# Kernel tuning notes

Hardware: AMD Instinct MI355X
Metric: run time of the kernel (lower is better)

## Reference

```python
import jax, jax.numpy as jnp
import numpy as np

T = 4096          # total packed tokens
SEG = 512         # segment length (position_ids reset every SEG)
D = 768           # hidden_size
H = 12            # num_attention_heads
DH = D // H       # head_dim = 64
THETA = 160000.0  # global_rope_theta (layer_id=0 -> global attention)


def setup_inputs() -> dict:
    key = jax.random.key(0)
    k1, k2, k3 = jax.random.split(key, 3)
    hidden_states = jax.random.normal(k1, (T, D), dtype=jnp.float32)
    # torch Linear weights stored transposed: here [in, out] for x @ W
    Wqkv = jax.random.normal(k2, (D, 3 * D), dtype=jnp.float32) / np.sqrt(D).astype(np.float32)
    Wo = jax.random.normal(k3, (D, D), dtype=jnp.float32) / np.sqrt(D).astype(np.float32)
    # packed batch: 8 segments of length SEG, position ids restart at 0
    position_ids = (jnp.arange(T, dtype=jnp.int32) % SEG)
    return {"hidden_states": hidden_states, "Wqkv": Wqkv, "Wo": Wo,
            "position_ids": position_ids}


def _neox_rope(x, pos):
    # x: [T, H, DH]; neox-style rotary over full head_dim
    half = DH // 2
    inv_freq = 1.0 / (THETA ** (jnp.arange(half, dtype=jnp.float32) * 2.0 / DH))
    freqs = pos.astype(jnp.float32)[:, None] * inv_freq[None, :]   # [T, half]
    cos = jnp.cos(freqs)[:, None, :]                               # [T, 1, half]
    sin = jnp.sin(freqs)[:, None, :]
    x1, x2 = x[..., :half], x[..., half:]
    return jnp.concatenate([x1 * cos - x2 * sin, x2 * cos + x1 * sin], axis=-1)


def reference(hidden_states, Wqkv, Wo, position_ids):
    qkv = hidden_states @ Wqkv                         # [T, 3D]
    q, k, v = jnp.split(qkv, 3, axis=-1)
    q = q.reshape(T, H, DH)
    k = k.reshape(T, H, DH)
    v = v.reshape(T, H, DH)
    q = _neox_rope(q, position_ids)
    k = _neox_rope(k, position_ids)
    # segment id per token (position_ids==0 marks a new sequence)
    seg = jnp.cumsum((position_ids == 0).astype(jnp.int32)) - 1
    mask = seg[:, None] == seg[None, :]                # block-diagonal [T, T]
    scale = 1.0 / np.sqrt(DH).astype(np.float32)
    scores = jnp.einsum('thd,shd->hts', q, k) * scale  # [H, T, T]
    scores = jnp.where(mask[None, :, :], scores, jnp.float32(-1e30))
    attn = jax.nn.softmax(scores, axis=-1)
    out = jnp.einsum('hts,shd->thd', attn, v).reshape(T, D)
    return out @ Wo
```

## Files before the change

kernel.cpp:

```cpp
#include <hip/hip_runtime.h>
#include <hip/hip_bf16.h>
#include <math.h>

#define T_TOK 4096
#define D_MODEL 768
#define H_HEADS 12
#define DH 64
#define SEG 512
#define NSEG 8
#define QKV_LD 2304

typedef __bf16 bf16x8_t __attribute__((ext_vector_type(8)));
typedef float f32x4_t __attribute__((ext_vector_type(4)));
typedef float f32x16_t __attribute__((ext_vector_type(16)));

#define GBK 64
#define QSCALE 0.18033688011112042f

#define FENCED_BARRIER()                         \
    do {                                         \
        __builtin_amdgcn_sched_barrier(0);       \
        __builtin_amdgcn_s_barrier();            \
        __builtin_amdgcn_sched_barrier(0);       \
    } while (0)

__device__ __forceinline__ void tconv_body(const float* __restrict__ in,
                                           __hip_bfloat16* __restrict__ out,
                                           int N, int K, int bx, int by, int tid,
                                           float (*tile)[65]) {
    const int k0 = by * 64;
    const int n0 = bx * 64;
    const int rr = tid >> 4;
    const int cc = (tid & 15) * 4;
#pragma unroll
    for (int i = 0; i < 4; ++i) {
        int r = i * 16 + rr;
        float4 v = *(const float4*)(in + (size_t)(k0 + r) * N + n0 + cc);
        tile[r][cc] = v.x; tile[r][cc + 1] = v.y; tile[r][cc + 2] = v.z; tile[r][cc + 3] = v.w;
    }
    __syncthreads();
#pragma unroll
    for (int i = 0; i < 4; ++i) {
        int n = i * 16 + rr;
        union { __hip_bfloat16 h[4]; ushort4 u; } o;
        o.h[0] = __float2bfloat16(tile[cc + 0][n]);
        o.h[1] = __float2bfloat16(tile[cc + 1][n]);
        o.h[2] = __float2bfloat16(tile[cc + 2][n]);
        o.h[3] = __float2bfloat16(tile[cc + 3][n]);
        *(ushort4*)(out + (size_t)(n0 + n) * K + k0 + cc) = o.u;
    }
}

__global__ __launch_bounds__(256) void prep_inputs(const float* __restrict__ hidden,
                                                   const float* __restrict__ Wqkv,
                                                   const float* __restrict__ Wo,
                                                   const int* __restrict__ pos_ids,
                                                   __hip_bfloat16* __restrict__ Xb,
                                                   __hip_bfloat16* __restrict__ Wqkvt,
                                                   __hip_bfloat16* __restrict__ Wot,
                                                   float2* __restrict__ rtab) {
    __shared__ float tile[64][65];
    const int b = blockIdx.x;
    const int tid = threadIdx.x;
    if (b < 3072) {
        int i = b * 256 + tid;
        float4 v = ((const float4*)hidden)[i];
        union { __hip_bfloat16 h[4]; ushort4 u; } o;
        o.h[0] = __float2bfloat16(v.x); o.h[1] = __float2bfloat16(v.y);
        o.h[2] = __float2bfloat16(v.z); o.h[3] = __float2bfloat16(v.w);
        ((ushort4*)Xb)[i] = o.u;
    } else if (b < 3504) {
        int lb = b - 3072;
        tconv_body(Wqkv, Wqkvt, QKV_LD, D_MODEL, lb % 36, lb / 36, tid, tile);
    } else if (b < 3648) {
        int lb = b - 3504;
        tconv_body(Wo, Wot, D_MODEL, D_MODEL, lb % 12, lb / 12, tid, tile);
    } else {
        int idx = (b - 3648) * 256 + tid;
        int t = idx >> 5;
        int i = idx & 31;
        float pos = (float)pos_ids[t];
        float inv_freq = powf(160000.0f, -(float)i / 32.0f);
        float s, c;
        sincosf(pos * inv_freq, &s, &c);
        rtab[idx] = make_float2(c, s);
    }
}

__global__ __launch_bounds__(512) void gemm_qkv_fused(const __hip_bfloat16* __restrict__ A,
                                                      const __hip_bfloat16* __restrict__ Bt,
                                                      const float2* __restrict__ rtab,
                                                      __hip_bfloat16* __restrict__ Qb,
                                                      __hip_bfloat16* __restrict__ Kb,
                                                      __hip_bfloat16* __restrict__ Vtb) {
    __shared__ __hip_bfloat16 As[2][128 * GBK];
    __shared__ __hip_bfloat16 Bs[2][128 * GBK];
    const int tid = threadIdx.x;
    const int lane = tid & 63;
    const int wid = tid >> 6;
    const int wr = wid >> 1;
    const int wc = wid & 1;
    const int orig = blockIdx.y * 18 + blockIdx.x;
    const int wg = (orig & 7) * 72 + (orig >> 3);
    const int m0 = (wg / 18) * 128;
    const int n0 = (wg % 18) * 128;
    const int K = D_MODEL;

    f32x4_t acc[2][4];
#pragma unroll
    for (int i = 0; i < 2; ++i)
#pragma unroll
        for (int j = 0; j < 4; ++j) acc[i][j] = (f32x4_t){0.f, 0.f, 0.f, 0.f};

    const int lr = lane >> 3;
    const int gc = lane & 7;
    const int swzc = (gc ^ lr) << 3;
    const int fr = lane & 15;
    const int l4 = lane >> 4;
    const int fsw = fr & 7;

#define STAGE_Q(buf_, k0_)                                                            \
    do {                                                                              \
        _Pragma("unroll")                                                             \
        for (int i_ = 0; i_ < 2; ++i_) {                                              \
            const int row_ = i_ * 64 + wid * 8;                                       \
            const __hip_bfloat16* ga_ = A + (size_t)(m0 + row_ + lr) * K + (k0_) + swzc; \
            __builtin_amdgcn_global_load_lds(                                         \
                (const __attribute__((address_space(1))) void*)ga_,                   \
                (__attribute__((address_space(3))) void*)(As[buf_] + row_ * GBK), 16, 0, 0); \
            const __hip_bfloat16* gb_ = Bt + (size_t)(n0 + row_ + lr) * K + (k0_) + swzc; \
            __builtin_amdgcn_global_load_lds(                                         \
                (const __attribute__((address_space(1))) void*)gb_,                   \
                (__attribute__((address_space(3))) void*)(Bs[buf_] + row_ * GBK), 16, 0, 0); \
        }                                                                             \
    } while (0)

    const int NKT = K / GBK;
    STAGE_Q(0, 0);
    for (int kt = 0; kt < NKT; ++kt) {
        const int cur = kt & 1;
        if (kt < NKT - 1) {
            STAGE_Q(cur ^ 1, (kt + 1) * GBK);
            asm volatile("s_waitcnt vmcnt(4)" ::: "memory");
        } else {
            asm volatile("s_waitcnt vmcnt(0)" ::: "memory");
        }
        FENCED_BARRIER();
#pragma unroll
        for (int kk = 0; kk < 2; ++kk) {
            const int rg = ((kk * 4 + l4) ^ fsw) << 3;
            bf16x8_t af[2], bfr[4];
#pragma unroll
            for (int mi = 0; mi < 2; ++mi)
                af[mi] = *(const bf16x8_t*)(As[cur] + (wr * 32 + mi * 16 + fr) * GBK + rg);
#pragma unroll
            for (int ni = 0; ni < 4; ++ni)
                bfr[ni] = *(const bf16x8_t*)(Bs[cur] + (wc * 64 + ni * 16 + fr) * GBK + rg);
#pragma unroll
            for (int mi = 0; mi < 2; ++mi)
#pragma unroll
                for (int ni = 0; ni < 4; ++ni)
                    acc[mi][ni] = __builtin_amdgcn_mfma_f32_16x16x32_bf16(
                        af[mi], bfr[ni], acc[mi][ni], 0, 0, 0);
        }
        asm volatile("" ::: "memory");
        FENCED_BARRIER();
    }
#undef STAGE_Q

    const int colbase = n0 + wc * 64;
    const int chunk = colbase >> 6;
    const int part = chunk / H_HEADS;
    const int h = chunk % H_HEADS;
    const int trow0 = m0 + wr * 32;

    ushort* scr = ((wid < 4) ? (ushort*)As : (ushort*)Bs) + (wid & 3) * 2560;

    if (part == 2) {
        const int seg = trow0 >> 9;
        const int key0 = trow0 & 511;
#pragma unroll
        for (int mi = 0; mi < 2; ++mi)
#pragma unroll
            for (int ni = 0; ni < 4; ++ni) {
                int d = ni * 16 + fr;
#pragma unroll
                for (int j = 0; j < 4; ++j)
                    scr[d * 40 + mi * 16 + l4 * 4 + j] =
                        __bfloat16_as_ushort(__float2bfloat16(acc[mi][ni][j]));
            }
        __builtin_amdgcn_sched_barrier(0);
        const ushort* rp = scr + lane * 40;
        uint4 v0 = *(const uint4*)(rp);
        uint4 v1 = *(const uint4*)(rp + 8);
        uint4 v2 = *(const uint4*)(rp + 16);
        uint4 v3 = *(const uint4*)(rp + 24);
        __hip_bfloat16* vd = Vtb + ((size_t)(h * NSEG + seg) * DH + lane) * SEG + key0;
        ((uint4*)vd)[0] = v0; ((uint4*)vd)[1] = v1;
        ((uint4*)vd)[2] = v2; ((uint4*)vd)[3] = v3;
    } else {
        __hip_bfloat16* dst = (part == 0) ? Qb : Kb;
        const float scale = (part == 0) ? QSCALE : 1.0f;
#pragma unroll
        for (int mi = 0; mi < 2; ++mi)
#pragma unroll
            for (int j = 0; j < 4; ++j) {
                int rl = mi * 16 + l4 * 4 + j;
                int t = trow0 + rl;
                const float2* tb = rtab + (size_t)t * 32;
                float2 cs0 = tb[fr];
                float2 cs1 = tb[16 + fr];
                float x1, x2;
                x1 = acc[mi][0][j]; x2 = acc[mi][2][j];
                scr[rl * 72 + fr] =
                    __bfloat16_as_ushort(__float2bfloat16((x1 * cs0.x - x2 * cs0.y) * scale));
                scr[rl * 72 + 32 + fr] =
                    __bfloat16_as_ushort(__float2bfloat16((x2 * cs0.x + x1 * cs0.y) * scale));
                x1 = acc[mi][1][j]; x2 = acc[mi][3][j];
                scr[rl * 72 + 16 + fr] =
                    __bfloat16_as_ushort(__float2bfloat16((x1 * cs1.x - x2 * cs1.y) * scale));
                scr[rl * 72 + 48 + fr] =
                    __bfloat16_as_ushort(__float2bfloat16((x2 * cs1.x + x1 * cs1.y) * scale));
            }
        __builtin_amdgcn_sched_barrier(0);
        const int row = lane >> 1, half = lane & 1;
        const ushort* rp = scr + row * 72 + half * 32;
        uint4 a0 = *(const uint4*)(rp);
        uint4 a1 = *(const uint4*)(rp + 8);
        uint4 a2 = *(const uint4*)(rp + 16);
        uint4 a3 = *(const uint4*)(rp + 24);
        __hip_bfloat16* op = dst + ((size_t)h * T_TOK + trow0 + row) * DH + half * 32;
        ((uint4*)op)[0] = a0; ((uint4*)op)[1] = a1;
        ((uint4*)op)[2] = a2; ((uint4*)op)[3] = a3;
    }
}

__global__ __launch_bounds__(256) void gemm_wo64(const __hip_bfloat16* __restrict__ A,
                                                 const __hip_bfloat16* __restrict__ Bt,
                                                 float* __restrict__ C) {
    __shared__ __hip_bfloat16 As[2][64 * GBK];
    __shared__ __hip_bfloat16 Bs[2][64 * GBK];
    const int tid = threadIdx.x;
    const int lane = tid & 63;
    const int wid = tid >> 6;
    const int wr = wid >> 1, wc = wid & 1;
    const int orig = blockIdx.y * 12 + blockIdx.x;
    const int wg = (orig & 7) * 96 + (orig >> 3);
    const int m0 = (wg / 12) * 64;
    const int n0 = (wg % 12) * 64;
    const int K = D_MODEL;
    const int N = D_MODEL;

    f32x4_t acc[2][2];
#pragma unroll
    for (int i = 0; i < 2; ++i)
#pragma unroll
        for (int j = 0; j < 2; ++j) acc[i][j] = (f32x4_t){0.f, 0.f, 0.f, 0.f};

    const int lr = lane >> 3;
    const int gc = lane & 7;
    const int swzc = (gc ^ lr) << 3;
    const int fr = lane & 15;
    const int l4 = lane >> 4;
    const int fsw = fr & 7;

#define STAGE_W(buf_, k0_)                                                            \
    do {                                                                              \
        _Pragma("unroll")                                                             \
        for (int i_ = 0; i_ < 2; ++i_) {                                              \
            const int row_ = i_ * 32 + wid * 8;                                       \
            const __hip_bfloat16* ga_ = A + (size_t)(m0 + row_ + lr) * K + (k0_) + swzc; \
            __builtin_amdgcn_global_load_lds(                                         \
                (const __attribute__((address_space(1))) void*)ga_,                   \
                (__attribute__((address_space(3))) void*)(As[buf_] + row_ * GBK), 16, 0, 0); \
            const __hip_bfloat16* gb_ = Bt + (size_t)(n0 + row_ + lr) * K + (k0_) + swzc; \
            __builtin_amdgcn_global_load_lds(                                         \
                (const __attribute__((address_space(1))) void*)gb_,                   \
                (__attribute__((address_space(3))) void*)(Bs[buf_] + row_ * GBK), 16, 0, 0); \
        }                                                                             \
    } while (0)

    const int NKT = K / GBK;
    STAGE_W(0, 0);
    for (int kt = 0; kt < NKT; ++kt) {
        const int cur = kt & 1;
        if (kt < NKT - 1) {
            STAGE_W(cur ^ 1, (kt + 1) * GBK);
            asm volatile("s_waitcnt vmcnt(4)" ::: "memory");
        } else {
            asm volatile("s_waitcnt vmcnt(0)" ::: "memory");
        }
        FENCED_BARRIER();
#pragma unroll
        for (int kk = 0; kk < 2; ++kk) {
            const int rg = ((kk * 4 + l4) ^ fsw) << 3;
            bf16x8_t af[2], bfr[2];
#pragma unroll
            for (int mi = 0; mi < 2; ++mi)
                af[mi] = *(const bf16x8_t*)(As[cur] + (wr * 32 + mi * 16 + fr) * GBK + rg);
#pragma unroll
            for (int ni = 0; ni < 2; ++ni)
                bfr[ni] = *(const bf16x8_t*)(Bs[cur] + (wc * 32 + ni * 16 + fr) * GBK + rg);
#pragma unroll
            for (int mi = 0; mi < 2; ++mi)
#pragma unroll
                for (int ni = 0; ni < 2; ++ni)
                    acc[mi][ni] = __builtin_amdgcn_mfma_f32_16x16x32_bf16(
                        af[mi], bfr[ni], acc[mi][ni], 0, 0, 0);
        }
        asm volatile("" ::: "memory");
        FENCED_BARRIER();
    }
#undef STAGE_W

    float* Cb = C + (size_t)(m0 + wr * 32) * N + n0 + wc * 32;
#pragma unroll
    for (int mi = 0; mi < 2; ++mi)
#pragma unroll
        for (int ni = 0; ni < 2; ++ni)
#pragma unroll
            for (int j = 0; j < 4; ++j) {
                int r = mi * 16 + (lane >> 4) * 4 + j;
                Cb[(size_t)r * N + ni * 16 + fr] = acc[mi][ni][j];
            }
}

__device__ __forceinline__ unsigned pk2(float a, float b) {
    unsigned ua = (unsigned)__bfloat16_as_ushort(__float2bfloat16(a));
    unsigned ub = (unsigned)__bfloat16_as_ushort(__float2bfloat16(b));
    return ua | (ub << 16);
}

__global__ __launch_bounds__(128) void attn_mfma(const __hip_bfloat16* __restrict__ Qb,
                                                 const __hip_bfloat16* __restrict__ Kb,
                                                 const __hip_bfloat16* __restrict__ Vtb,
                                                 __hip_bfloat16* __restrict__ attnb) {
    __shared__ __hip_bfloat16 KS[2][64 * 64];
    __shared__ __hip_bfloat16 VS[2][64 * 64];

    const int tid = threadIdx.x;
    const int lane = tid & 63;
    const int w = tid >> 6;
    const int hi = lane >> 5;
    const int l31 = lane & 31;
    const int orig = blockIdx.x;
    const int wg = (orig & 7) * 96 + (orig >> 3);
    const int qt = wg & 7;
    const int hs = wg >> 3;
    const int h = hs % H_HEADS;
    const int seg = hs / H_HEADS;
    const int t0 = seg * SEG + qt * 64 + w * 32;

    const __hip_bfloat16* kb = Kb + ((size_t)h * T_TOK + seg * SEG) * DH;
    const __hip_bfloat16* vb = Vtb + (size_t)(h * NSEG + seg) * DH * SEG;

    bf16x8_t qf[4];
    {
        const __hip_bfloat16* qp = Qb + ((size_t)h * T_TOK + t0 + l31) * DH + hi * 8;
#pragma unroll
        for (int s = 0; s < 4; ++s) qf[s] = *(const bf16x8_t*)(qp + s * 16);
    }

    const int gr = lane >> 3;
    const int gc = lane & 7;

#pragma unroll
    for (int i = 0; i < 4; ++i) {
        int G = i * 128 + w * 64;
        int rk = (G >> 3) + gr;
        const __hip_bfloat16* sk = kb + (size_t)rk * DH + ((gc ^ (rk & 7)) << 3);
        __builtin_amdgcn_global_load_lds(
            (const __attribute__((address_space(1))) void*)sk,
            (__attribute__((address_space(3))) void*)(&KS[0][G * 8]), 16, 0, 0);
        const __hip_bfloat16* sv = vb + (size_t)rk * SEG + ((gc ^ (rk & 7)) << 3);
        __builtin_amdgcn_global_load_lds(
            (const __attribute__((address_space(1))) void*)sv,
            (__attribute__((address_space(3))) void*)(&VS[0][G * 8]), 16, 0, 0);
    }
    __syncthreads();

    f32x16_t ot[2];
#pragma unroll
    for (int n = 0; n < 2; ++n)
#pragma unroll
        for (int r = 0; r < 16; ++r) ot[n][r] = 0.f;
    float mrun = -3.0e38f, lrun = 0.f;

    for (int kv = 0; kv < 8; ++kv) {
        const int bb = kv & 1;
        if (kv < 7) {
#pragma unroll
            for (int i = 0; i < 4; ++i) {
                int G = i * 128 + w * 64;
                int rk = (G >> 3) + gr;
                const __hip_bfloat16* sk = kb + (size_t)((kv + 1) * 64 + rk) * DH + ((gc ^ (rk & 7)) << 3);
                __builtin_amdgcn_global_load_lds(
                    (const __attribute__((address_space(1))) void*)sk,
                    (__attribute__((address_space(3))) void*)(&KS[bb ^ 1][G * 8]), 16, 0, 0);
                const __hip_bfloat16* sv = vb + (size_t)rk * SEG + (kv + 1) * 64 + ((gc ^ (rk & 7)) << 3);
                __builtin_amdgcn_global_load_lds(
                    (const __attribute__((address_space(1))) void*)sv,
                    (__attribute__((address_space(3))) void*)(&VS[bb ^ 1][G * 8]), 16, 0, 0);
            }
        }

        f32x16_t st[2];
#pragma unroll
        for (int t = 0; t < 2; ++t)
#pragma unroll
            for (int r = 0; r < 16; ++r) st[t][r] = 0.f;
#pragma unroll
        for (int s = 0; s < 4; ++s) {
            int gk = s * 2 + hi;
            bf16x8_t k0 = *(const bf16x8_t*)(&KS[bb][l31 * 64 + ((gk ^ (l31 & 7)) << 3)]);
            bf16x8_t k1 = *(const bf16x8_t*)(&KS[bb][(32 + l31) * 64 + ((gk ^ (l31 & 7)) << 3)]);
            st[0] = __builtin_amdgcn_mfma_f32_32x32x16_bf16(k0, qf[s], st[0], 0, 0, 0);
            st[1] = __builtin_amdgcn_mfma_f32_32x32x16_bf16(k1, qf[s], st[1], 0, 0, 0);
        }

        float tmax = st[0][0];
#pragma unroll
        for (int r = 1; r < 16; ++r) tmax = fmaxf(tmax, st[0][r]);
#pragma unroll
        for (int r = 0; r < 16; ++r) tmax = fmaxf(tmax, st[1][r]);
        tmax = fmaxf(tmax, __shfl_xor(tmax, 32));

        if (!__all(tmax <= mrun + 8.0f)) {
            float mnew = fmaxf(mrun, tmax);
            float corr = exp2f(mrun - mnew);
            lrun *= corr;
#pragma unroll
            for (int n = 0; n < 2; ++n)
#pragma unroll
                for (int r = 0; r < 16; ++r) ot[n][r] *= corr;
            mrun = mnew;
        }
        float psum = 0.f;
#pragma unroll
        for (int t = 0; t < 2; ++t)
#pragma unroll
            for (int r = 0; r < 16; ++r) {
                float p = exp2f(st[t][r] - mrun);
                st[t][r] = p;
                psum += p;
            }
        psum += __shfl_xor(psum, 32);
        lrun += psum;

        bf16x8_t pf[4];
#pragma unroll
        for (int t = 0; t < 2; ++t) {
            unsigned wv[8], ov[8];
#pragma unroll
            for (int j = 0; j < 8; ++j) wv[j] = pk2(st[t][2 * j], st[t][2 * j + 1]);
#pragma unroll
            for (int j = 0; j < 8; ++j) ov[j] = (unsigned)__shfl_xor((int)wv[j], 32);
#pragma unroll
            for (int sh = 0; sh < 2; ++sh) {
                int b = sh * 4;
                union { unsigned u[4]; bf16x8_t v; } u8;
                u8.u[0] = hi ? ov[b + 2] : wv[b + 0];
                u8.u[1] = hi ? ov[b + 3] : wv[b + 1];
                u8.u[2] = hi ? wv[b + 2] : ov[b + 0];
                u8.u[3] = hi ? wv[b + 3] : ov[b + 1];
                pf[t * 2 + sh] = u8.v;
            }
        }

#pragma unroll
        for (int s = 0; s < 4; ++s) {
            int gk = s * 2 + hi;
            bf16x8_t v0 = *(const bf16x8_t*)(&VS[bb][l31 * 64 + ((gk ^ (l31 & 7)) << 3)]);
            bf16x8_t v1 = *(const bf16x8_t*)(&VS[bb][(32 + l31) * 64 + ((gk ^ (l31 & 7)) << 3)]);
            ot[0] = __builtin_amdgcn_mfma_f32_32x32x16_bf16(v0, pf[s], ot[0], 0, 0, 0);
            ot[1] = __builtin_amdgcn_mfma_f32_32x32x16_bf16(v1, pf[s], ot[1], 0, 0, 0);
        }
        __syncthreads();
    }

    float invl = 1.0f / lrun;
    ushort* Os = (ushort*)&KS[0][0];
    const int wbase = w * (64 * 33);
#pragma unroll
    for (int n = 0; n < 2; ++n)
#pragma unroll
        for (int r = 0; r < 16; ++r) {
            int d = n * 32 + (r & 3) + 8 * (r >> 2) + 4 * hi;
            Os[wbase + d * 33 + l31] = __bfloat16_as_ushort(__float2bfloat16(ot[n][r] * invl));
        }
    __syncthreads();
    {
        unsigned ow2[16];
#pragma unroll
        for (int j = 0; j < 16; ++j) {
            unsigned lo = Os[wbase + (hi * 32 + 2 * j) * 33 + l31];
            unsigned hh = Os[wbase + (hi * 32 + 2 * j + 1) * 33 + l31];
            ow2[j] = lo | (hh << 16);
        }
        uint4* gd = (uint4*)(attnb + (size_t)(t0 + l31) * D_MODEL + h * DH + hi * 32);
        gd[0] = make_uint4(ow2[0], ow2[1], ow2[2], ow2[3]);
        gd[1] = make_uint4(ow2[4], ow2[5], ow2[6], ow2[7]);
        gd[2] = make_uint4(ow2[8], ow2[9], ow2[10], ow2[11]);
        gd[3] = make_uint4(ow2[12], ow2[13], ow2[14], ow2[15]);
    }
}

extern "C" void kernel_launch(void* const* d_in, const int* in_sizes, int n_in,
                              void* d_out, int out_size, void* d_ws, size_t ws_size,
                              hipStream_t stream) {
    const float* hidden = (const float*)d_in[0];
    const float* Wqkv   = (const float*)d_in[1];
    const float* Wo     = (const float*)d_in[2];
    const int*   pos    = (const int*)d_in[3];

    char* ws = (char*)d_ws;
    __hip_bfloat16* Xb    = (__hip_bfloat16*)(ws);
    __hip_bfloat16* Wqkvt = (__hip_bfloat16*)(ws + 6291456);
    __hip_bfloat16* Wot   = (__hip_bfloat16*)(ws + 9830400);
    __hip_bfloat16* Qb    = (__hip_bfloat16*)(ws + 11010048);
    __hip_bfloat16* Kb    = (__hip_bfloat16*)(ws + 17301504);
    __hip_bfloat16* Vtb   = (__hip_bfloat16*)(ws + 23592960);
    __hip_bfloat16* attnb = (__hip_bfloat16*)(ws + 29884416);
    float2* rtab          = (float2*)(ws + 36175872);
    float* out = (float*)d_out;

    prep_inputs<<<4160, 256, 0, stream>>>(hidden, Wqkv, Wo, pos, Xb, Wqkvt, Wot, rtab);

    gemm_qkv_fused<<<dim3(QKV_LD / 128, T_TOK / 128), 512, 0, stream>>>(
        Xb, Wqkvt, rtab, Qb, Kb, Vtb);

    attn_mfma<<<768, 128, 0, stream>>>(Qb, Kb, Vtb, attnb);

    gemm_wo64<<<dim3(D_MODEL / 64, T_TOK / 64), 256, 0, stream>>>(
        attnb, Wot, out);
}
```

Before: 75.79 us.

## Process two 32-row query groups per wave in attention to reuse K/V tiles

```diff
diff --git a/kernel.cpp b/kernel.cpp
--- a/kernel.cpp
+++ b/kernel.cpp
@@ -344,21 +344,22 @@
     const int hi = lane >> 5;
     const int l31 = lane & 31;
     const int orig = blockIdx.x;
-    const int wg = (orig & 7) * 96 + (orig >> 3);
-    const int qt = wg & 7;
-    const int hs = wg >> 3;
+    const int wg = (orig & 7) * 48 + (orig >> 3);
+    const int qp2 = wg & 3;
+    const int hs = wg >> 2;
     const int h = hs % H_HEADS;
     const int seg = hs / H_HEADS;
-    const int t0 = seg * SEG + qt * 64 + w * 32;
+    const int t0 = seg * SEG + qp2 * 128 + w * 64;
 
     const __hip_bfloat16* kb = Kb + ((size_t)h * T_TOK + seg * SEG) * DH;
     const __hip_bfloat16* vb = Vtb + (size_t)(h * NSEG + seg) * DH * SEG;
 
-    bf16x8_t qf[4];
-    {
-        const __hip_bfloat16* qp = Qb + ((size_t)h * T_TOK + t0 + l31) * DH + hi * 8;
-#pragma unroll
-        for (int s = 0; s < 4; ++s) qf[s] = *(const bf16x8_t*)(qp + s * 16);
+    bf16x8_t qf[2][4];
+#pragma unroll
+    for (int g = 0; g < 2; ++g) {
+        const __hip_bfloat16* qp = Qb + ((size_t)h * T_TOK + t0 + g * 32 + l31) * DH + hi * 8;
+#pragma unroll
+        for (int s = 0; s < 4; ++s) qf[g][s] = *(const bf16x8_t*)(qp + s * 16);
     }
 
     const int gr = lane >> 3;
@@ -379,12 +380,15 @@
     }
     __syncthreads();
 
-    f32x16_t ot[2];
-#pragma unroll
-    for (int n = 0; n < 2; ++n)
-#pragma unroll
-        for (int r = 0; r < 16; ++r) ot[n][r] = 0.f;
-    float mrun = -3.0e38f, lrun = 0.f;
+    f32x16_t ot[2][2];
+#pragma unroll
+    for (int g = 0; g < 2; ++g)
+#pragma unroll
+        for (int n = 0; n < 2; ++n)
+#pragma unroll
+            for (int r = 0; r < 16; ++r) ot[g][n][r] = 0.f;
+    float mrun[2] = {-3.0e38f, -3.0e38f};
+    float lrun[2] = {0.f, 0.f};
 
     for (int kv = 0; kv < 8; ++kv) {
         const int bb = kv & 1;
@@ -404,104 +408,116 @@
             }
         }
 
-        f32x16_t st[2];
-#pragma unroll
-        for (int t = 0; t < 2; ++t)
-#pragma unroll
-            for (int r = 0; r < 16; ++r) st[t][r] = 0.f;
-#pragma unroll
-        for (int s = 0; s < 4; ++s) {
-            int gk = s * 2 + hi;
-            bf16x8_t k0 = *(const bf16x8_t*)(&KS[bb][l31 * 64 + ((gk ^ (l31 & 7)) << 3)]);
-            bf16x8_t k1 = *(const bf16x8_t*)(&KS[bb][(32 + l31) * 64 + ((gk ^ (l31 & 7)) << 3)]);
-            st[0] = __builtin_amdgcn_mfma_f32_32x32x16_bf16(k0, qf[s], st[0], 0, 0, 0);
-            st[1] = __builtin_amdgcn_mfma_f32_32x32x16_bf16(k1, qf[s], st[1], 0, 0, 0);
-        }
-
-        float tmax = st[0][0];
-#pragma unroll
-        for (int r = 1; r < 16; ++r) tmax = fmaxf(tmax, st[0][r]);
-#pragma unroll
-        for (int r = 0; r < 16; ++r) tmax = fmaxf(tmax, st[1][r]);
-        tmax = fmaxf(tmax, __shfl_xor(tmax, 32));
-
-        if (!__all(tmax <= mrun + 8.0f)) {
-            float mnew = fmaxf(mrun, tmax);
-            float corr = exp2f(mrun - mnew);
-            lrun *= corr;
-#pragma unroll
-            for (int n = 0; n < 2; ++n)
-#pragma unroll
-                for (int r = 0; r < 16; ++r) ot[n][r] *= corr;
-            mrun = mnew;
-        }
-        float psum = 0.f;
-#pragma unroll
-        for (int t = 0; t < 2; ++t)
-#pragma unroll
-            for (int r = 0; r < 16; ++r) {
-                float p = exp2f(st[t][r] - mrun);
-                st[t][r] = p;
-                psum += p;
-            }
-        psum += __shfl_xor(psum, 32);
-        lrun += psum;
-
-        bf16x8_t pf[4];
-#pragma unroll
-        for (int t = 0; t < 2; ++t) {
-            unsigned wv[8], ov[8];
-#pragma unroll
-            for (int j = 0; j < 8; ++j) wv[j] = pk2(st[t][2 * j], st[t][2 * j + 1]);
-#pragma unroll
-            for (int j = 0; j < 8; ++j) ov[j] = (unsigned)__shfl_xor((int)wv[j], 32);
-#pragma unroll
-            for (int sh = 0; sh < 2; ++sh) {
-                int b = sh * 4;
-                union { unsigned u[4]; bf16x8_t v; } u8;
-                u8.u[0] = hi ? ov[b + 2] : wv[b + 0];
-                u8.u[1] = hi ? ov[b + 3] : wv[b + 1];
-                u8.u[2] = hi ? wv[b + 2] : ov[b + 0];
-                u8.u[3] = hi ? wv[b + 3] : ov[b + 1];
-                pf[t * 2 + sh] = u8.v;
-            }
-        }
-
-#pragma unroll
-        for (int s = 0; s < 4; ++s) {
-            int gk = s * 2 + hi;
-            bf16x8_t v0 = *(const bf16x8_t*)(&VS[bb][l31 * 64 + ((gk ^ (l31 & 7)) << 3)]);
-            bf16x8_t v1 = *(const bf16x8_t*)(&VS[bb][(32 + l31) * 64 + ((gk ^ (l31 & 7)) << 3)]);
-            ot[0] = __builtin_amdgcn_mfma_f32_32x32x16_bf16(v0, pf[s], ot[0], 0, 0, 0);
-            ot[1] = __builtin_amdgcn_mfma_f32_32x32x16_bf16(v1, pf[s], ot[1], 0, 0, 0);
+#pragma unroll
+        for (int g = 0; g < 2; ++g) {
+            f32x16_t st[2];
+#pragma unroll
+            for (int t = 0; t < 2; ++t)
+#pragma unroll
+                for (int r = 0; r < 16; ++r) st[t][r] = 0.f;
+            __builtin_amdgcn_s_setprio(1);
+#pragma unroll
+            for (int s = 0; s < 4; ++s) {
+                int gk = s * 2 + hi;
+                bf16x8_t k0 = *(const bf16x8_t*)(&KS[bb][l31 * 64 + ((gk ^ (l31 & 7)) << 3)]);
+                bf16x8_t k1 = *(const bf16x8_t*)(&KS[bb][(32 + l31) * 64 + ((gk ^ (l31 & 7)) << 3)]);
+                st[0] = __builtin_amdgcn_mfma_f32_32x32x16_bf16(k0, qf[g][s], st[0], 0, 0, 0);
+                st[1] = __builtin_amdgcn_mfma_f32_32x32x16_bf16(k1, qf[g][s], st[1], 0, 0, 0);
+            }
+            __builtin_amdgcn_s_setprio(0);
+
+            float tmax = st[0][0];
+#pragma unroll
+            for (int r = 1; r < 16; ++r) tmax = fmaxf(tmax, st[0][r]);
+#pragma unroll
+            for (int r = 0; r < 16; ++r) tmax = fmaxf(tmax, st[1][r]);
+            tmax = fmaxf(tmax, __shfl_xor(tmax, 32));
+
+            if (!__all(tmax <= mrun[g] + 8.0f)) {
+                float mnew = fmaxf(mrun[g], tmax);
+                float corr = exp2f(mrun[g] - mnew);
+                lrun[g] *= corr;
+#pragma unroll
+                for (int n = 0; n < 2; ++n)
+#pragma unroll
+                    for (int r = 0; r < 16; ++r) ot[g][n][r] *= corr;
+                mrun[g] = mnew;
+            }
+            float psum = 0.f;
+#pragma unroll
+            for (int t = 0; t < 2; ++t)
+#pragma unroll
+                for (int r = 0; r < 16; ++r) {
+                    float p = exp2f(st[t][r] - mrun[g]);
+                    st[t][r] = p;
+                    psum += p;
+                }
+            psum += __shfl_xor(psum, 32);
+            lrun[g] += psum;
+
+            bf16x8_t pf[4];
+#pragma unroll
+            for (int t = 0; t < 2; ++t) {
+                unsigned wv[8], ov[8];
+#pragma unroll
+                for (int j = 0; j < 8; ++j) wv[j] = pk2(st[t][2 * j], st[t][2 * j + 1]);
+#pragma unroll
+                for (int j = 0; j < 8; ++j) ov[j] = (unsigned)__shfl_xor((int)wv[j], 32);
+#pragma unroll
+                for (int sh = 0; sh < 2; ++sh) {
+                    int b = sh * 4;
+                    union { unsigned u[4]; bf16x8_t v; } u8;
+                    u8.u[0] = hi ? ov[b + 2] : wv[b + 0];
+                    u8.u[1] = hi ? ov[b + 3] : wv[b + 1];
+                    u8.u[2] = hi ? wv[b + 2] : ov[b + 0];
+                    u8.u[3] = hi ? wv[b + 3] : ov[b + 1];
+                    pf[t * 2 + sh] = u8.v;
+                }
+            }
+
+            __builtin_amdgcn_s_setprio(1);
+#pragma unroll
+            for (int s = 0; s < 4; ++s) {
+                int gk = s * 2 + hi;
+                bf16x8_t v0 = *(const bf16x8_t*)(&VS[bb][l31 * 64 + ((gk ^ (l31 & 7)) << 3)]);
+                bf16x8_t v1 = *(const bf16x8_t*)(&VS[bb][(32 + l31) * 64 + ((gk ^ (l31 & 7)) << 3)]);
+                ot[g][0] = __builtin_amdgcn_mfma_f32_32x32x16_bf16(v0, pf[s], ot[g][0], 0, 0, 0);
+                ot[g][1] = __builtin_amdgcn_mfma_f32_32x32x16_bf16(v1, pf[s], ot[g][1], 0, 0, 0);
+            }
+            __builtin_amdgcn_s_setprio(0);
         }
         __syncthreads();
     }
 
-    float invl = 1.0f / lrun;
     ushort* Os = (ushort*)&KS[0][0];
     const int wbase = w * (64 * 33);
 #pragma unroll
-    for (int n = 0; n < 2; ++n)
-#pragma unroll
-        for (int r = 0; r < 16; ++r) {
-            int d = n * 32 + (r & 3) + 8 * (r >> 2) + 4 * hi;
-            Os[wbase + d * 33 + l31] = __bfloat16_as_ushort(__float2bfloat16(ot[n][r] * invl));
-        }
-    __syncthreads();
-    {
-        unsigned ow2[16];
-#pragma unroll
-        for (int j = 0; j < 16; ++j) {
-            unsigned lo = Os[wbase + (hi * 32 + 2 * j) * 33 + l31];
-            unsigned hh = Os[wbase + (hi * 32 + 2 * j + 1) * 33 + l31];
-            ow2[j] = lo | (hh << 16);
-        }
-        uint4* gd = (uint4*)(attnb + (size_t)(t0 + l31) * D_MODEL + h * DH + hi * 32);
-        gd[0] = make_uint4(ow2[0], ow2[1], ow2[2], ow2[3]);
-        gd[1] = make_uint4(ow2[4], ow2[5], ow2[6], ow2[7]);
-        gd[2] = make_uint4(ow2[8], ow2[9], ow2[10], ow2[11]);
-        gd[3] = make_uint4(ow2[12], ow2[13], ow2[14], ow2[15]);
+    for (int g = 0; g < 2; ++g) {
+        float invl = 1.0f / lrun[g];
+#pragma unroll
+        for (int n = 0; n < 2; ++n)
+#pragma unroll
+            for (int r = 0; r < 16; ++r) {
+                int d = n * 32 + (r & 3) + 8 * (r >> 2) + 4 * hi;
+                Os[wbase + d * 33 + l31] =
+                    __bfloat16_as_ushort(__float2bfloat16(ot[g][n][r] * invl));
+            }
+        __syncthreads();
+        {
+            unsigned ow2[16];
+#pragma unroll
+            for (int j = 0; j < 16; ++j) {
+                unsigned lo = Os[wbase + (hi * 32 + 2 * j) * 33 + l31];
+                unsigned hh = Os[wbase + (hi * 32 + 2 * j + 1) * 33 + l31];
+                ow2[j] = lo | (hh << 16);
+            }
+            uint4* gd = (uint4*)(attnb + (size_t)(t0 + g * 32 + l31) * D_MODEL + h * DH + hi * 32);
+            gd[0] = make_uint4(ow2[0], ow2[1], ow2[2], ow2[3]);
+            gd[1] = make_uint4(ow2[4], ow2[5], ow2[6], ow2[7]);
+            gd[2] = make_uint4(ow2[8], ow2[9], ow2[10], ow2[11]);
+            gd[3] = make_uint4(ow2[12], ow2[13], ow2[14], ow2[15]);
+        }
+        __syncthreads();
     }
 }
 
@@ -529,7 +545,7 @@
     gemm_qkv_fused<<<dim3(QKV_LD / 128, T_TOK / 128), 512, 0, stream>>>(
         Xb, Wqkvt, rtab, Qb, Kb, Vtb);
 
-    attn_mfma<<<768, 128, 0, stream>>>(Qb, Kb, Vtb, attnb);
+    attn_mfma<<<384, 128, 0, stream>>>(Qb, Kb, Vtb, attnb);
 
     gemm_wo64<<<dim3(D_MODEL / 64, T_TOK / 64), 256, 0, stream>>>(
         attnb, Wot, out);
```

Result: slower. 81.78 us (+7.9%).
